# Kernel tuning notes

Measured on AMD Instinct MI355X. Metric: run time of the kernel, lower is better.

The kernel has to match this reference:

```python
import jax, jax.numpy as jnp
import numpy as np

HIDDEN = 1024
NUM_HEADS = 16
HEAD_DIM = HIDDEN // NUM_HEADS


def setup_inputs() -> dict:
    key = jax.random.key(0)
    k1, k2, k3, k4, k5 = jax.random.split(key, 5)
    B, S, T, H = 2, 2048, 2048, HIDDEN
    scale = 0.02
    return {
        "query": jax.random.normal(k1, (B, S, H), dtype=jnp.float32),
        "key_value": jax.random.normal(k2, (B, T, H), dtype=jnp.float32),
        "Wq": jax.random.normal(k3, (H, H), dtype=jnp.float32) * scale,
        "Wkv": jax.random.normal(k4, (H, 2 * H), dtype=jnp.float32) * scale,
        "Wc": jax.random.normal(k5, (H, H), dtype=jnp.float32) * scale,
    }


def reference(query, key_value, Wq, Wkv, Wc):
    B, S, H = query.shape
    T = key_value.shape[1]
    nh, hd = NUM_HEADS, HEAD_DIM

    q = query @ Wq                                  # [B,S,H]
    kv = key_value @ Wkv                            # [B,T,2H]
    k, v = kv[..., :H], kv[..., H:]

    # [B, nh, S|T, hd]
    q = q.reshape(B, S, nh, hd).transpose(0, 2, 1, 3)
    k = k.reshape(B, T, nh, hd).transpose(0, 2, 1, 3)
    v = v.reshape(B, T, nh, hd).transpose(0, 2, 1, 3)

    scale = hd ** -0.5
    scores = jnp.einsum("bhsd,bhtd->bhst", q * scale, k)   # [B,nh,S,T]
    probs = jax.nn.softmax(scores, axis=-1)
    y = jnp.einsum("bhst,bhtd->bhsd", probs, v)             # [B,nh,S,hd]
    y = y.transpose(0, 2, 1, 3).reshape(B, S, H)
    return y @ Wc
```

## Files before the change

kernel.cpp:

```cpp
#include <hip/hip_runtime.h>
#include <hip/hip_bf16.h>


typedef unsigned short u16;
typedef __attribute__((ext_vector_type(4))) float float4v;
typedef __attribute__((ext_vector_type(4))) unsigned short u16x4;
typedef __attribute__((ext_vector_type(8))) short short8;
typedef __attribute__((ext_vector_type(4))) float floatx4;

__device__ __forceinline__ u16 f2bf(float f) {
  unsigned u = __float_as_uint(f);
  u += 0x7fffu + ((u >> 16) & 1u);
  return (u16)(u >> 16);
}

__device__ __forceinline__ float fast_exp2(float x) {
#if __has_builtin(__builtin_amdgcn_exp2f)
  return __builtin_amdgcn_exp2f(x);
#else
  return exp2f(x);
#endif
}

__device__ __forceinline__ void store_out(float* p, float v) { *p = v; }
__device__ __forceinline__ void store_out(u16* p, float v) { *p = f2bf(v); }

__device__ __forceinline__ void gld16(const void* g, void* l) {
  __builtin_amdgcn_global_load_lds(
      (const __attribute__((address_space(1))) void*)g,
      (__attribute__((address_space(3))) void*)l, 16, 0, 0);
}

__device__ __forceinline__ unsigned pack_bf2(float a, float b) {
  unsigned ua = __float_as_uint(a) + 0x8000u;
  unsigned ub = __float_as_uint(b) + 0x8000u;
  return __builtin_amdgcn_perm(ub, ua, 0x07060302u);
}

__global__ void cvt_bf16_2(const float* __restrict__ a, const float* __restrict__ b,
                           u16* __restrict__ oa, u16* __restrict__ ob, int n4) {
  int i = blockIdx.x * blockDim.x + threadIdx.x;
  if (i >= n4) return;
  const float* src = blockIdx.y ? b : a;
  u16* dst = blockIdx.y ? ob : oa;
  float4v v = ((const float4v*)src)[i];
  u16x4 o;
  o.x = f2bf(v.x); o.y = f2bf(v.y); o.z = f2bf(v.z); o.w = f2bf(v.w);
  ((u16x4*)dst)[i] = o;
}

__global__ void transpose_cvt(const float* __restrict__ in, u16* __restrict__ out,
                              int R, int C) {
  __shared__ float tile[32][33];
  int bx = blockIdx.x * 32;
  int by = blockIdx.y * 32;
  int tx = threadIdx.x, ty = threadIdx.y;
#pragma unroll
  for (int i = 0; i < 32; i += 8)
    tile[ty + i][tx] = in[(size_t)(by + ty + i) * C + bx + tx];
  __syncthreads();
#pragma unroll
  for (int i = 0; i < 32; i += 8)
    out[(size_t)(bx + ty + i) * R + by + tx] = f2bf(tile[tx][ty + i]);
}

template <typename OutT, int NI>
__device__ __forceinline__ void gemm_body(const u16* __restrict__ A,
                                          const u16* __restrict__ Bt,
                                          OutT* __restrict__ C,
                                          int N, int K, float scale,
                                          int bm, int bn,
                                          u16* As, u16* Bs) {
  const int t = threadIdx.x;
  const int w = t >> 6, l = t & 63;
  const int lane15 = l & 15, quad = l >> 4;
  const int wm = w >> 1, wn = w & 1;
  const int x3 = lane15 & 3;
  const int BSZ = NI * 1024;

  const int srow = t >> 2;
  const int scol = (((t & 3) ^ (srow & 3)) << 3);
  const u16* ag0 = A + (size_t)(bm + srow) * K + scol;
  const u16* ag1 = ag0 + (size_t)64 * K;
  const u16* bg0 = Bt + (size_t)(bn + srow) * K + scol;
  const u16* bg1 = bg0 + (size_t)64 * K;

  int afo[4], bfo[NI];
#pragma unroll
  for (int mi = 0; mi < 4; ++mi)
    afo[mi] = (wm * 64 + mi * 16 + lane15) * 32 + ((quad ^ x3) << 3);
#pragma unroll
  for (int ni = 0; ni < NI; ++ni)
    bfo[ni] = (wn * (NI * 16) + ni * 16 + lane15) * 32 + ((quad ^ x3) << 3);

  floatx4 acc[4][NI] = {};

  auto stage = [&](int kt, int ab, int bb) {
    gld16(ag0 + kt, &As[ab + t * 8]);
    gld16(ag1 + kt, &As[ab + 2048 + t * 8]);
    gld16(bg0 + kt, &Bs[bb + t * 8]);
    if (NI == 4) gld16(bg1 + kt, &Bs[bb + 2048 + t * 8]);
  };
  auto compute = [&](int ab, int bb) {
    short8 af[4], bf[NI];
#pragma unroll
    for (int mi = 0; mi < 4; ++mi) af[mi] = *(const short8*)&As[ab + afo[mi]];
#pragma unroll
    for (int ni = 0; ni < NI; ++ni) bf[ni] = *(const short8*)&Bs[bb + bfo[ni]];
#pragma unroll
    for (int mi = 0; mi < 4; ++mi)
#pragma unroll
      for (int ni = 0; ni < NI; ++ni)
        acc[mi][ni] = __builtin_amdgcn_mfma_f32_16x16x32_bf16(af[mi], bf[ni],
                                                              acc[mi][ni], 0, 0, 0);
  };

  stage(0, 0, 0);
  __syncthreads();
  for (int kt = 0; kt < K; kt += 64) {
    if (kt + 32 < K) stage(kt + 32, 4096, BSZ);
    compute(0, 0);
    __syncthreads();
    if (kt + 64 < K) stage(kt + 64, 0, 0);
    compute(4096, BSZ);
    __syncthreads();
  }

#pragma unroll
  for (int mi = 0; mi < 4; ++mi)
#pragma unroll
    for (int ni = 0; ni < NI; ++ni) {
      int col = bn + wn * (NI * 16) + ni * 16 + lane15;
#pragma unroll
      for (int r = 0; r < 4; ++r) {
        int row = bm + wm * 64 + mi * 16 + quad * 4 + r;
        store_out(&C[(size_t)row * N + col], acc[mi][ni][r] * scale);
      }
    }
}

__global__ __launch_bounds__(256) void gemm_qkv(const u16* __restrict__ qin,
                                                const u16* __restrict__ kvin,
                                                const u16* __restrict__ Wqt,
                                                const u16* __restrict__ Wkvt,
                                                u16* __restrict__ qp,
                                                u16* __restrict__ kvp,
                                                float qscale) {
  __shared__ __align__(16) u16 As[2 * 4096];
  __shared__ __align__(16) u16 Bs[2 * 4096];
  const bool isq = blockIdx.x < 8;
  const u16* A = isq ? qin : kvin;
  const u16* Bt = isq ? Wqt : Wkvt;
  u16* C = isq ? qp : kvp;
  const int N = isq ? 1024 : 2048;
  const int bn = (isq ? blockIdx.x : blockIdx.x - 8) * 128;
  const float scale = isq ? qscale : 1.0f;
  gemm_body<u16, 4>(A, Bt, C, N, 1024, scale, blockIdx.y * 128, bn, As, Bs);
}

__global__ __launch_bounds__(256) void gemm_out(const u16* __restrict__ A,
                                                const u16* __restrict__ Bt,
                                                float* __restrict__ C) {
  __shared__ __align__(16) u16 As[2 * 4096];
  __shared__ __align__(16) u16 Bs[2 * 2048];
  gemm_body<float, 2>(A, Bt, C, 1024, 1024, 1.0f, blockIdx.y * 128,
                      blockIdx.x * 64, As, Bs);
}

__global__ __launch_bounds__(256) void transpose_v(const u16* __restrict__ KV,
                                                   u16* __restrict__ VT) {
  __shared__ __align__(16) u16 tile[64 * 72];
  const int bh = blockIdx.y, b = bh >> 4, h = bh & 15;
  const int t0 = blockIdx.x * 64;
  const int t = threadIdx.x;
#pragma unroll
  for (int c = t; c < 512; c += 256) {
    int row = c >> 3, col8 = (c & 7) << 3;
    *(short8*)&tile[row * 72 + col8] =
        *(const short8*)&KV[(size_t)(b * 2048 + t0 + row) * 2048 + 1024 + h * 64 + col8];
  }
  __syncthreads();
#pragma unroll
  for (int c = t; c < 512; c += 256) {
    int d = c >> 3, t8 = (c & 7) << 3;
    short8 v;
#pragma unroll
    for (int j = 0; j < 8; ++j) v[j] = (short)tile[(t8 + j) * 72 + d];
    *(short8*)&VT[(size_t)(bh * 64 + d) * 2048 + t0 + t8] = v;
  }
}

__global__ __launch_bounds__(256) void attn_kern(const u16* __restrict__ Q,
                                                 const u16* __restrict__ KV,
                                                 const u16* __restrict__ VT,
                                                 u16* __restrict__ Y) {
  __shared__ __align__(16) u16 Ks[2 * 4096];
  __shared__ __align__(16) u16 VTs[2 * 4096];
  __shared__ __align__(16) u16 Ps[4096];
  const int t = threadIdx.x, w = t >> 6, l = t & 63;
  const int lane15 = l & 15, quad = l >> 4;
  const int bh = blockIdx.y, b = bh >> 4, h = bh & 15;
  const int qrow0 = b * 2048 + blockIdx.x * 64;
  const int xm = lane15 & 7;

  short8 qf[2];
#pragma unroll
  for (int ks = 0; ks < 2; ++ks)
    qf[ks] = *(const short8*)&Q[(size_t)(qrow0 + w * 16 + lane15) * 1024 +
                                h * 64 + ks * 32 + quad * 8];

  floatx4 yacc[4] = {};
  float lrun = 0.f;

  const int srow = t >> 3;
  const int scol = (((t & 7) ^ (srow & 7)) << 3);
  const u16* kg = KV + (size_t)(b * 2048 + srow) * 2048 + h * 64 + scol;
  const u16* vg = VT + (size_t)(bh * 64 + srow) * 2048 + scol;

  const int prow = (w * 16 + lane15) * 64;
  int kfo[2][4], vfo[2][4], pwo[4], pro[2];
#pragma unroll
  for (int ks = 0; ks < 2; ++ks)
#pragma unroll
    for (int ti = 0; ti < 4; ++ti)
      kfo[ks][ti] = (ti * 16 + lane15) * 64 + (((ks * 4 + quad) ^ xm) << 3);
#pragma unroll
  for (int ts = 0; ts < 2; ++ts) {
#pragma unroll
    for (int ni = 0; ni < 4; ++ni)
      vfo[ts][ni] = (ni * 16 + lane15) * 64 + (((ts * 4 + quad) ^ xm) << 3);
    pro[ts] = prow + (((ts * 4 + quad) ^ xm) << 3);
  }
#pragma unroll
  for (int ti = 0; ti < 4; ++ti)
    pwo[ti] = prow + (((ti * 2 + (quad >> 1)) ^ xm) << 3) + ((quad & 1) << 2);

  auto stage = [&](int t0n, int buf) {
    const u16* kgn = kg + (size_t)t0n * 2048;
    gld16(kgn, &Ks[buf + t * 8]);
    gld16(kgn + (size_t)32 * 2048, &Ks[buf + 2048 + t * 8]);
    const u16* vgn = vg + t0n;
    gld16(vgn, &VTs[buf + t * 8]);
    gld16(vgn + (size_t)32 * 2048, &VTs[buf + 2048 + t * 8]);
  };
  auto compute = [&](int buf) {
    floatx4 sacc[4] = {};
#pragma unroll
    for (int ks = 0; ks < 2; ++ks)
#pragma unroll
      for (int ti = 0; ti < 4; ++ti) {
        short8 kf = *(const short8*)&Ks[buf + kfo[ks][ti]];
        sacc[ti] = __builtin_amdgcn_mfma_f32_16x16x32_bf16(kf, qf[ks], sacc[ti], 0, 0, 0);
      }
    float s = 0.f;
#pragma unroll
    for (int ti = 0; ti < 4; ++ti) {
      float p0 = fast_exp2(sacc[ti][0]);
      float p1 = fast_exp2(sacc[ti][1]);
      float p2 = fast_exp2(sacc[ti][2]);
      float p3 = fast_exp2(sacc[ti][3]);
      s += (p0 + p1) + (p2 + p3);
      uint2 pk;
      pk.x = pack_bf2(p0, p1);
      pk.y = pack_bf2(p2, p3);
      *(uint2*)&Ps[pwo[ti]] = pk;
    }
    s += __shfl_xor(s, 16);
    s += __shfl_xor(s, 32);
    lrun += s;
#pragma unroll
    for (int ts = 0; ts < 2; ++ts) {
      short8 pf = *(const short8*)&Ps[pro[ts]];
#pragma unroll
      for (int ni = 0; ni < 4; ++ni) {
        short8 vf = *(const short8*)&VTs[buf + vfo[ts][ni]];
        yacc[ni] = __builtin_amdgcn_mfma_f32_16x16x32_bf16(pf, vf, yacc[ni], 0, 0, 0);
      }
    }
  };

  stage(0, 0);
  __syncthreads();
  for (int t0 = 0; t0 < 2048; t0 += 128) {
    if (t0 + 64 < 2048) stage(t0 + 64, 4096);
    compute(0);
    __syncthreads();
    if (t0 + 128 < 2048) stage(t0 + 128, 0);
    compute(4096);
    __syncthreads();
  }

  float linv = 1.0f / lrun;
  float lB[4];
#pragma unroll
  for (int r = 0; r < 4; ++r)
    lB[r] = __shfl(linv, (quad << 4) | (quad * 4 + r));
#pragma unroll
  for (int ni = 0; ni < 4; ++ni)
#pragma unroll
    for (int r = 0; r < 4; ++r) {
      int row = qrow0 + w * 16 + quad * 4 + r;
      Y[(size_t)row * 1024 + h * 64 + ni * 16 + lane15] = f2bf(yacc[ni][r] * lB[r]);
    }
}

extern "C" void kernel_launch(void* const* d_in, const int* in_sizes, int n_in,
                              void* d_out, int out_size, void* d_ws, size_t ws_size,
                              hipStream_t stream) {
  const float* query = (const float*)d_in[0];
  const float* key_value = (const float*)d_in[1];
  const float* Wq = (const float*)d_in[2];
  const float* Wkv = (const float*)d_in[3];
  const float* Wc = (const float*)d_in[4];
  float* out = (float*)d_out;

  const size_t MB = 1024 * 1024;
  char* ws = (char*)d_ws;
  u16* qin  = (u16*)(ws + 0 * MB);
  u16* kvin = (u16*)(ws + 8 * MB);
  u16* Wqt  = (u16*)(ws + 16 * MB);
  u16* Wkvt = (u16*)(ws + 18 * MB);
  u16* Wct  = (u16*)(ws + 22 * MB);
  u16* qp   = (u16*)(ws + 24 * MB);
  u16* kvp  = (u16*)(ws + 32 * MB);
  u16* vt   = (u16*)(ws + 48 * MB);
  u16* y    = (u16*)(ws + 56 * MB);

  const int nAct4 = 2 * 2048 * 1024 / 4;
  cvt_bf16_2<<<dim3(nAct4 / 256, 2), dim3(256), 0, stream>>>(query, key_value,
                                                             qin, kvin, nAct4);
  transpose_cvt<<<dim3(32, 32), dim3(32, 8), 0, stream>>>(Wq, Wqt, 1024, 1024);
  transpose_cvt<<<dim3(64, 32), dim3(32, 8), 0, stream>>>(Wkv, Wkvt, 1024, 2048);
  transpose_cvt<<<dim3(32, 32), dim3(32, 8), 0, stream>>>(Wc, Wct, 1024, 1024);

  const float qscale = 0.125f * 1.4426950408889634f;
  gemm_qkv<<<dim3(24, 32), dim3(256), 0, stream>>>(qin, kvin, Wqt, Wkvt, qp, kvp, qscale);
  transpose_v<<<dim3(32, 32), dim3(256), 0, stream>>>(kvp, vt);
  attn_kern<<<dim3(32, 32), dim3(256), 0, stream>>>(qp, kvp, vt, y);
  gemm_out<<<dim3(16, 32), dim3(256), 0, stream>>>(y, Wct, out);
}
```

Measured before the change: 219.4 us.

## Widen attention blocks, split-K output GEMM, merge weight transposes, MFMA row sums

Attention now runs 512-thread blocks over 128 query rows, so each staged K/V tile serves twice as many queries. The softmax denominator is accumulated with an MFMA against a vector of ones instead of shuffles. The three weight transpose kernels are merged into one launch. The output GEMM uses 128x128 tiles split-K in two halves plus a separate add kernel. Packed bf16 conversion uses the hardware cvt_pk builtin when it is available. Together these cut redundant loads and launches, at the cost of an extra fp32 pass over the output and higher LDS use per block.

```diff
diff --git a/kernel.cpp b/kernel.cpp
--- a/kernel.cpp
+++ b/kernel.cpp
@@ -22,6 +22,19 @@
 #endif
 }
 
+__device__ __forceinline__ unsigned pack_bf2(float a, float b) {
+#if __has_builtin(__builtin_amdgcn_cvt_pk_bf16_f32)
+  auto r = __builtin_amdgcn_cvt_pk_bf16_f32(a, b);
+  unsigned u;
+  __builtin_memcpy(&u, &r, 4);
+  return u;
+#else
+  unsigned ua = __float_as_uint(a) + 0x8000u;
+  unsigned ub = __float_as_uint(b) + 0x8000u;
+  return __builtin_amdgcn_perm(ub, ua, 0x07060302u);
+#endif
+}
+
 __device__ __forceinline__ void store_out(float* p, float v) { *p = v; }
 __device__ __forceinline__ void store_out(u16* p, float v) { *p = f2bf(v); }
 
@@ -29,12 +42,6 @@
   __builtin_amdgcn_global_load_lds(
       (const __attribute__((address_space(1))) void*)g,
       (__attribute__((address_space(3))) void*)l, 16, 0, 0);
-}
-
-__device__ __forceinline__ unsigned pack_bf2(float a, float b) {
-  unsigned ua = __float_as_uint(a) + 0x8000u;
-  unsigned ub = __float_as_uint(b) + 0x8000u;
-  return __builtin_amdgcn_perm(ub, ua, 0x07060302u);
 }
 
 __global__ void cvt_bf16_2(const float* __restrict__ a, const float* __restrict__ b,
@@ -49,10 +56,19 @@
   ((u16x4*)dst)[i] = o;
 }
 
-__global__ void transpose_cvt(const float* __restrict__ in, u16* __restrict__ out,
-                              int R, int C) {
+__global__ void transpose_cvt3(const float* __restrict__ Wq,
+                               const float* __restrict__ Wkv,
+                               const float* __restrict__ Wc,
+                               u16* __restrict__ Wqt, u16* __restrict__ Wkvt,
+                               u16* __restrict__ Wct) {
   __shared__ float tile[32][33];
+  const int z = blockIdx.z;
+  const float* in = z == 0 ? Wq : (z == 1 ? Wkv : Wc);
+  u16* out = z == 0 ? Wqt : (z == 1 ? Wkvt : Wct);
+  const int C = (z == 1) ? 2048 : 1024;
+  const int R = 1024;
   int bx = blockIdx.x * 32;
+  if (bx >= C) return;
   int by = blockIdx.y * 32;
   int tx = threadIdx.x, ty = threadIdx.y;
 #pragma unroll
@@ -68,7 +84,7 @@
 __device__ __forceinline__ void gemm_body(const u16* __restrict__ A,
                                           const u16* __restrict__ Bt,
                                           OutT* __restrict__ C,
-                                          int N, int K, float scale,
+                                          int N, int lda, int Klen, float scale,
                                           int bm, int bn,
                                           u16* As, u16* Bs) {
   const int t = threadIdx.x;
@@ -80,10 +96,10 @@
 
   const int srow = t >> 2;
   const int scol = (((t & 3) ^ (srow & 3)) << 3);
-  const u16* ag0 = A + (size_t)(bm + srow) * K + scol;
-  const u16* ag1 = ag0 + (size_t)64 * K;
-  const u16* bg0 = Bt + (size_t)(bn + srow) * K + scol;
-  const u16* bg1 = bg0 + (size_t)64 * K;
+  const u16* ag0 = A + (size_t)(bm + srow) * lda + scol;
+  const u16* ag1 = ag0 + (size_t)64 * lda;
+  const u16* bg0 = Bt + (size_t)(bn + srow) * lda + scol;
+  const u16* bg1 = bg0 + (size_t)64 * lda;
 
   int afo[4], bfo[NI];
 #pragma unroll
@@ -117,11 +133,11 @@
 
   stage(0, 0, 0);
   __syncthreads();
-  for (int kt = 0; kt < K; kt += 64) {
-    if (kt + 32 < K) stage(kt + 32, 4096, BSZ);
+  for (int kt = 0; kt < Klen; kt += 64) {
+    if (kt + 32 < Klen) stage(kt + 32, 4096, BSZ);
     compute(0, 0);
     __syncthreads();
-    if (kt + 64 < K) stage(kt + 64, 0, 0);
+    if (kt + 64 < Klen) stage(kt + 64, 0, 0);
     compute(4096, BSZ);
     __syncthreads();
   }
@@ -155,16 +171,28 @@
   const int N = isq ? 1024 : 2048;
   const int bn = (isq ? blockIdx.x : blockIdx.x - 8) * 128;
   const float scale = isq ? qscale : 1.0f;
-  gemm_body<u16, 4>(A, Bt, C, N, 1024, scale, blockIdx.y * 128, bn, As, Bs);
+  gemm_body<u16, 4>(A, Bt, C, N, 1024, 1024, scale, blockIdx.y * 128, bn, As, Bs);
 }
 
 __global__ __launch_bounds__(256) void gemm_out(const u16* __restrict__ A,
                                                 const u16* __restrict__ Bt,
-                                                float* __restrict__ C) {
+                                                float* __restrict__ P0,
+                                                float* __restrict__ P1) {
   __shared__ __align__(16) u16 As[2 * 4096];
-  __shared__ __align__(16) u16 Bs[2 * 2048];
-  gemm_body<float, 2>(A, Bt, C, 1024, 1024, 1.0f, blockIdx.y * 128,
-                      blockIdx.x * 64, As, Bs);
+  __shared__ __align__(16) u16 Bs[2 * 4096];
+  const int k0 = blockIdx.z * 512;
+  float* dst = blockIdx.z ? P1 : P0;
+  gemm_body<float, 4>(A + k0, Bt + k0, dst, 1024, 1024, 512, 1.0f,
+                      blockIdx.y * 128, blockIdx.x * 128, As, Bs);
+}
+
+__global__ void add_f32(float* __restrict__ out, const float* __restrict__ p1, int n4) {
+  int i = blockIdx.x * blockDim.x + threadIdx.x;
+  if (i >= n4) return;
+  float4v a = ((const float4v*)out)[i];
+  float4v b = ((const float4v*)p1)[i];
+  a.x += b.x; a.y += b.y; a.z += b.z; a.w += b.w;
+  ((float4v*)out)[i] = a;
 }
 
 __global__ __launch_bounds__(256) void transpose_v(const u16* __restrict__ KV,
@@ -190,17 +218,17 @@
   }
 }
 
-__global__ __launch_bounds__(256) void attn_kern(const u16* __restrict__ Q,
+__global__ __launch_bounds__(512) void attn_kern(const u16* __restrict__ Q,
                                                  const u16* __restrict__ KV,
                                                  const u16* __restrict__ VT,
                                                  u16* __restrict__ Y) {
   __shared__ __align__(16) u16 Ks[2 * 4096];
   __shared__ __align__(16) u16 VTs[2 * 4096];
-  __shared__ __align__(16) u16 Ps[4096];
+  __shared__ __align__(16) u16 Ps[8192];
   const int t = threadIdx.x, w = t >> 6, l = t & 63;
   const int lane15 = l & 15, quad = l >> 4;
   const int bh = blockIdx.y, b = bh >> 4, h = bh & 15;
-  const int qrow0 = b * 2048 + blockIdx.x * 64;
+  const int qrow0 = b * 2048 + blockIdx.x * 128;
   const int xm = lane15 & 7;
 
   short8 qf[2];
@@ -209,8 +237,11 @@
     qf[ks] = *(const short8*)&Q[(size_t)(qrow0 + w * 16 + lane15) * 1024 +
                                 h * 64 + ks * 32 + quad * 8];
 
+  const short8 vones = {0x3F80, 0x3F80, 0x3F80, 0x3F80,
+                        0x3F80, 0x3F80, 0x3F80, 0x3F80};
+
   floatx4 yacc[4] = {};
-  float lrun = 0.f;
+  floatx4 lacc = {};
 
   const int srow = t >> 3;
   const int scol = (((t & 7) ^ (srow & 7)) << 3);
@@ -236,12 +267,8 @@
     pwo[ti] = prow + (((ti * 2 + (quad >> 1)) ^ xm) << 3) + ((quad & 1) << 2);
 
   auto stage = [&](int t0n, int buf) {
-    const u16* kgn = kg + (size_t)t0n * 2048;
-    gld16(kgn, &Ks[buf + t * 8]);
-    gld16(kgn + (size_t)32 * 2048, &Ks[buf + 2048 + t * 8]);
-    const u16* vgn = vg + t0n;
-    gld16(vgn, &VTs[buf + t * 8]);
-    gld16(vgn + (size_t)32 * 2048, &VTs[buf + 2048 + t * 8]);
+    gld16(kg + (size_t)t0n * 2048, &Ks[buf + t * 8]);
+    gld16(vg + t0n, &VTs[buf + t * 8]);
   };
   auto compute = [&](int buf) {
     floatx4 sacc[4] = {};
@@ -252,25 +279,21 @@
         short8 kf = *(const short8*)&Ks[buf + kfo[ks][ti]];
         sacc[ti] = __builtin_amdgcn_mfma_f32_16x16x32_bf16(kf, qf[ks], sacc[ti], 0, 0, 0);
       }
-    float s = 0.f;
 #pragma unroll
     for (int ti = 0; ti < 4; ++ti) {
       float p0 = fast_exp2(sacc[ti][0]);
       float p1 = fast_exp2(sacc[ti][1]);
       float p2 = fast_exp2(sacc[ti][2]);
       float p3 = fast_exp2(sacc[ti][3]);
-      s += (p0 + p1) + (p2 + p3);
       uint2 pk;
       pk.x = pack_bf2(p0, p1);
       pk.y = pack_bf2(p2, p3);
       *(uint2*)&Ps[pwo[ti]] = pk;
     }
-    s += __shfl_xor(s, 16);
-    s += __shfl_xor(s, 32);
-    lrun += s;
 #pragma unroll
     for (int ts = 0; ts < 2; ++ts) {
       short8 pf = *(const short8*)&Ps[pro[ts]];
+      lacc = __builtin_amdgcn_mfma_f32_16x16x32_bf16(pf, vones, lacc, 0, 0, 0);
 #pragma unroll
       for (int ni = 0; ni < 4; ++ni) {
         short8 vf = *(const short8*)&VTs[buf + vfo[ts][ni]];
@@ -290,18 +313,14 @@
     __syncthreads();
   }
 
-  float linv = 1.0f / lrun;
-  float lB[4];
-#pragma unroll
-  for (int r = 0; r < 4; ++r)
-    lB[r] = __shfl(linv, (quad << 4) | (quad * 4 + r));
-#pragma unroll
-  for (int ni = 0; ni < 4; ++ni)
-#pragma unroll
-    for (int r = 0; r < 4; ++r) {
-      int row = qrow0 + w * 16 + quad * 4 + r;
-      Y[(size_t)row * 1024 + h * 64 + ni * 16 + lane15] = f2bf(yacc[ni][r] * lB[r]);
-    }
+#pragma unroll
+  for (int r = 0; r < 4; ++r) {
+    float linv = 1.0f / lacc[r];
+    int row = qrow0 + w * 16 + quad * 4 + r;
+#pragma unroll
+    for (int ni = 0; ni < 4; ++ni)
+      Y[(size_t)row * 1024 + h * 64 + ni * 16 + lane15] = f2bf(yacc[ni][r] * linv);
+  }
 }
 
 extern "C" void kernel_launch(void* const* d_in, const int* in_sizes, int n_in,
@@ -325,17 +344,18 @@
   u16* kvp  = (u16*)(ws + 32 * MB);
   u16* vt   = (u16*)(ws + 48 * MB);
   u16* y    = (u16*)(ws + 56 * MB);
+  float* p1 = (float*)(ws + 0 * MB);
 
   const int nAct4 = 2 * 2048 * 1024 / 4;
   cvt_bf16_2<<<dim3(nAct4 / 256, 2), dim3(256), 0, stream>>>(query, key_value,
                                                              qin, kvin, nAct4);
-  transpose_cvt<<<dim3(32, 32), dim3(32, 8), 0, stream>>>(Wq, Wqt, 1024, 1024);
-  transpose_cvt<<<dim3(64, 32), dim3(32, 8), 0, stream>>>(Wkv, Wkvt, 1024, 2048);
-  transpose_cvt<<<dim3(32, 32), dim3(32, 8), 0, stream>>>(Wc, Wct, 1024, 1024);
+  transpose_cvt3<<<dim3(64, 32, 3), dim3(32, 8), 0, stream>>>(Wq, Wkv, Wc,
+                                                              Wqt, Wkvt, Wct);
 
   const float qscale = 0.125f * 1.4426950408889634f;
   gemm_qkv<<<dim3(24, 32), dim3(256), 0, stream>>>(qin, kvin, Wqt, Wkvt, qp, kvp, qscale);
   transpose_v<<<dim3(32, 32), dim3(256), 0, stream>>>(kvp, vt);
-  attn_kern<<<dim3(32, 32), dim3(256), 0, stream>>>(qp, kvp, vt, y);
-  gemm_out<<<dim3(16, 32), dim3(256), 0, stream>>>(y, Wct, out);
-}
+  attn_kern<<<dim3(16, 32), dim3(512), 0, stream>>>(qp, kvp, vt, y);
+  gemm_out<<<dim3(8, 32, 2), dim3(256), 0, stream>>>(y, Wct, out, p1);
+  add_f32<<<dim3(nAct4 / 256), dim3(256), 0, stream>>>(out, p1, nAct4);
+}
```

After: 211.8 us. 3.4% less time.
